# Kernel tuning notes

Hardware: AMD Instinct MI355X
Metric: run time of the kernel (lower is better)

The kernel has to match this reference:

```python
import jax, jax.numpy as jnp
import numpy as np

B, N, H, O = 262144, 64, 256, 64
MAX_ITER = 30
TOL = 1e-7
NU = 1.0


def setup_inputs() -> dict:
    key = jax.random.key(0)
    kx, kr, k1, k2, k3, k4 = jax.random.split(key, 6)
    x = jax.random.normal(kx, (B, N), dtype=jnp.float32) * 3.0
    r = jax.random.uniform(kr, (N,), dtype=jnp.float32) + 0.5  # positive rates in [0.5, 1.5)
    # MLP params (torch Linear: y = x @ W.T + b), Kaiming-ish scaling
    W1 = jax.random.normal(k1, (H, N), dtype=jnp.float32) * (1.0 / np.sqrt(N))
    b1 = jax.random.normal(k2, (H,), dtype=jnp.float32) * 0.01
    W2 = jax.random.normal(k3, (O, H), dtype=jnp.float32) * (1.0 / np.sqrt(H))
    b2 = jax.random.normal(k4, (O,), dtype=jnp.float32) * 0.01
    return {"x": x, "r": r, "W1": W1, "b1": b1, "W2": W2, "b2": b2}


def _solve_s(x, r):
    """Vectorized Newton solve of sum_i e^{-2 r_i s} x_i^2 = 1 per sample.

    Replicates solve_s_single: s starts at 0, up to MAX_ITER Newton steps,
    frozen once |F(s)| < TOL; all-zero samples return s = 0.
    """
    x2 = x * x  # [B, N]
    zero_mask = jnp.all(jnp.abs(x) <= 1e-12, axis=1)  # torch.allclose(x, 0, atol=1e-12)

    def body(_, s):
        e = jnp.exp(-2.0 * r[None, :] * s[:, None])        # [B, N]
        val = jnp.sum(e * x2, axis=1) - 1.0                # F(s)     [B]
        dval = jnp.sum(-2.0 * r[None, :] * e * x2, axis=1) # F'(s)    [B]
        safe_d = jnp.where(dval == 0.0, 1.0, dval)
        step = val / safe_d
        step = jnp.where((jnp.abs(val) < TOL) | zero_mask, 0.0, step)
        return s - step

    s0 = jnp.zeros(x.shape[0], dtype=x.dtype)
    return jax.lax.fori_loop(0, MAX_ITER, body, s0)


def reference(x, r, W1, b1, W2, b2):
    S = _solve_s(x, r)[:, None]                 # [B, 1], detached in torch (built via .item())
    S = jax.lax.stop_gradient(S)
    x_sphere = x * jnp.exp(-r[None, :] * S)     # d(-s) x
    h = jnp.maximum(x_sphere @ W1.T + b1, 0.0)  # [B, H]
    mlp_out = h @ W2.T + b2                     # [B, O]
    return mlp_out * jnp.exp(NU * S)
```

## Files before the change

kernel.cpp:

```cpp
#include <hip/hip_runtime.h>

typedef __attribute__((ext_vector_type(8))) short short8;
typedef __attribute__((ext_vector_type(4))) float floatx4;

static __device__ __forceinline__ unsigned short f2bf(float f) {
    unsigned u = __float_as_uint(f);
    u += 0x7FFFu + ((u >> 16) & 1u);
    return (unsigned short)(u >> 16);
}

__global__ __launch_bounds__(256) void convert_w_k(const float* __restrict__ W1,
                                                   const float* __restrict__ W2,
                                                   unsigned short* __restrict__ w1b,
                                                   unsigned short* __restrict__ w2b) {
    int i = blockIdx.x * 256 + threadIdx.x;
    w1b[i] = f2bf(W1[i]);
    w2b[i] = f2bf(W2[i]);
}

__global__ __launch_bounds__(256) void newton_k(const float* __restrict__ x,
                                                const float* __restrict__ r,
                                                unsigned short* __restrict__ xs,
                                                float* __restrict__ scl) {
    int tid = blockIdx.x * 256 + threadIdx.x;
    int sample = tid >> 2;
    int part = tid & 3;

    const float4* x4 = (const float4*)(x + (size_t)sample * 64 + part * 16);
    const float4* r4 = (const float4*)(r + part * 16);
    float xv[16], rr[16], x2[16], rx2[16];
#pragma unroll
    for (int j = 0; j < 4; ++j) {
        float4 a = x4[j];
        float4 b = r4[j];
        xv[4 * j + 0] = a.x; xv[4 * j + 1] = a.y; xv[4 * j + 2] = a.z; xv[4 * j + 3] = a.w;
        rr[4 * j + 0] = b.x; rr[4 * j + 1] = b.y; rr[4 * j + 2] = b.z; rr[4 * j + 3] = b.w;
    }

    float sum0 = 0.f, sumr = 0.f;
    int nz = 0;
#pragma unroll
    for (int j = 0; j < 16; ++j) {
        x2[j] = xv[j] * xv[j];
        rx2[j] = rr[j] * x2[j];
        sum0 += x2[j];
        sumr += rx2[j];
        nz |= (fabsf(xv[j]) > 1e-12f) ? 1 : 0;
    }
    sum0 += __shfl_xor(sum0, 1); sum0 += __shfl_xor(sum0, 2);
    sumr += __shfl_xor(sumr, 1); sumr += __shfl_xor(sumr, 2);
    nz   |= __shfl_xor(nz, 1);   nz   |= __shfl_xor(nz, 2);

    float s = 0.f;
    if (nz) {
        s = __logf(sum0) * sum0 / (2.f * sumr);
#pragma unroll 1
        for (int it = 0; it < 11; ++it) {
            float m2s = -2.f * s;
            float v = 0.f, dv = 0.f;
#pragma unroll
            for (int j = 0; j < 16; ++j) {
                float e = __expf(m2s * rr[j]);
                v = fmaf(e, x2[j], v);
                dv = fmaf(e, rx2[j], dv);
            }
            v += __shfl_xor(v, 1);   v += __shfl_xor(v, 2);
            dv += __shfl_xor(dv, 1); dv += __shfl_xor(dv, 2);
            float val = v - 1.f;
            s += val / (2.f * dv);
        }
    }

    unsigned up[8];
#pragma unroll
    for (int j = 0; j < 8; ++j) {
        float a = xv[2 * j] * __expf(-s * rr[2 * j]);
        float b = xv[2 * j + 1] * __expf(-s * rr[2 * j + 1]);
        up[j] = (unsigned)f2bf(a) | ((unsigned)f2bf(b) << 16);
    }
    uint4* dst = (uint4*)(xs + (size_t)sample * 64 + part * 16);
    dst[0] = make_uint4(up[0], up[1], up[2], up[3]);
    dst[1] = make_uint4(up[4], up[5], up[6], up[7]);
    if (part == 0) scl[sample] = __expf(s);
}

__global__ __launch_bounds__(256, 2) void mlp_k(const unsigned short* __restrict__ xs,
                                                const float* __restrict__ scl,
                                                const unsigned short* __restrict__ w1b,
                                                const unsigned short* __restrict__ w2b,
                                                const float* __restrict__ b1,
                                                const float* __restrict__ b2,
                                                float* __restrict__ out,
                                                int tiles_per_block) {
    __shared__ unsigned short sW1[256 * 64];
    __shared__ unsigned short sW2[64 * 256];
    __shared__ unsigned short sH[64 * 64];

    int tid = threadIdx.x;

    const uint4* w1u = (const uint4*)w1b;
#pragma unroll
    for (int c = 0; c < 8; ++c) {
        int g = tid + c * 256;
        int row = g >> 3, ch = g & 7;
        *(uint4*)&sW1[row * 64 + (ch ^ (row & 7)) * 8] = w1u[g];
    }
    const uint4* w2u = (const uint4*)w2b;
#pragma unroll
    for (int c = 0; c < 8; ++c) {
        int g = tid + c * 256;
        int row = g >> 5, ch = g & 31;
        *(uint4*)&sW2[row * 256 + (ch ^ (row & 7)) * 8] = w2u[g];
    }
    __syncthreads();

    int wave = tid >> 6, lane = tid & 63;
    int q = lane >> 4, l16 = lane & 15;
    int sx = l16 & 7;

    float bias1[16];
#pragma unroll
    for (int n = 0; n < 16; ++n) bias1[n] = b1[n * 16 + l16];
    float bias2[4];
#pragma unroll
    for (int n = 0; n < 4; ++n) bias2[n] = b2[n * 16 + l16];

    for (int tt = 0; tt < tiles_per_block; ++tt) {
        size_t m0 = ((size_t)blockIdx.x * tiles_per_block + tt) * 64;
        int myrow = wave * 16 + l16;

        const short8* xrow = (const short8*)(xs + (m0 + myrow) * 64);
        short8 a0 = xrow[q];
        short8 a1 = xrow[q + 4];
        float sc[4];
#pragma unroll
        for (int reg = 0; reg < 4; ++reg) sc[reg] = scl[m0 + wave * 16 + q * 4 + reg];

        floatx4 oacc[4];
#pragma unroll
        for (int n = 0; n < 4; ++n) oacc[n] = (floatx4){0.f, 0.f, 0.f, 0.f};

#pragma unroll
        for (int hc = 0; hc < 4; ++hc) {
#pragma unroll
            for (int n = 0; n < 4; ++n) {
                int hcol = hc * 4 + n;
                int row = hcol * 16 + l16;
                short8 wb0 = *(const short8*)&sW1[row * 64 + (q ^ sx) * 8];
                short8 wb1 = *(const short8*)&sW1[row * 64 + ((q + 4) ^ sx) * 8];
                floatx4 acc = {0.f, 0.f, 0.f, 0.f};
                acc = __builtin_amdgcn_mfma_f32_16x16x32_bf16(a0, wb0, acc, 0, 0, 0);
                acc = __builtin_amdgcn_mfma_f32_16x16x32_bf16(a1, wb1, acc, 0, 0, 0);
                float bias = bias1[hcol];
#pragma unroll
                for (int reg = 0; reg < 4; ++reg) {
                    float h = acc[reg] + bias;
                    h = h > 0.f ? h : 0.f;
                    int rr = wave * 16 + q * 4 + reg;
                    int E = n * 16 + l16;
                    sH[rr * 64 + (((E >> 3) ^ (rr & 7)) * 8) + (E & 7)] = f2bf(h);
                }
            }
            short8 ha0 = *(const short8*)&sH[myrow * 64 + (q ^ sx) * 8];
            short8 ha1 = *(const short8*)&sH[myrow * 64 + ((q + 4) ^ sx) * 8];
#pragma unroll
            for (int n = 0; n < 4; ++n) {
                int row = n * 16 + l16;
                short8 wb0 = *(const short8*)&sW2[row * 256 + (hc * 8 + (q ^ sx)) * 8];
                short8 wb1 = *(const short8*)&sW2[row * 256 + (hc * 8 + ((q + 4) ^ sx)) * 8];
                oacc[n] = __builtin_amdgcn_mfma_f32_16x16x32_bf16(ha0, wb0, oacc[n], 0, 0, 0);
                oacc[n] = __builtin_amdgcn_mfma_f32_16x16x32_bf16(ha1, wb1, oacc[n], 0, 0, 0);
            }
        }
#pragma unroll
        for (int n = 0; n < 4; ++n) {
#pragma unroll
            for (int reg = 0; reg < 4; ++reg) {
                float o = (oacc[n][reg] + bias2[n]) * sc[reg];
                out[(m0 + wave * 16 + q * 4 + reg) * 64 + n * 16 + l16] = o;
            }
        }
    }
}

extern "C" void kernel_launch(void* const* d_in, const int* in_sizes, int n_in,
                              void* d_out, int out_size, void* d_ws, size_t ws_size,
                              hipStream_t stream) {
    const float* x  = (const float*)d_in[0];
    const float* r  = (const float*)d_in[1];
    const float* W1 = (const float*)d_in[2];
    const float* b1 = (const float*)d_in[3];
    const float* W2 = (const float*)d_in[4];
    const float* b2 = (const float*)d_in[5];
    float* out = (float*)d_out;
    int B = in_sizes[0] / 64;

    char* ws = (char*)d_ws;
    unsigned short* w1b = (unsigned short*)ws;
    unsigned short* w2b = (unsigned short*)(ws + 32768);
    float* scl = (float*)(ws + 65536);
    unsigned short* xs = (unsigned short*)(ws + 65536 + (size_t)B * 4);

    convert_w_k<<<64, 256, 0, stream>>>(W1, W2, w1b, w2b);
    newton_k<<<B / 64, 256, 0, stream>>>(x, r, xs, scl);

    int tiles = B / 64;
    int blocks = 512;
    int tpb = tiles / blocks;
    mlp_k<<<blocks, 256, 0, stream>>>(xs, scl, w1b, w2b, b1, b2, out, tpb);
}
```

Baseline: 168.5 us.

## Fuse Newton solve into MLP kernel and drop bf16 intermediate buffer

Merges the per-sample Newton solve into the MLP kernel. Each wave now computes the scaled input rows for its own 16 samples, writes them to a shared-memory tile that is reused for the hidden activations, and passes the exp(s) scale through lane shuffles. This removes the global write and re-read of the bf16 intermediate and the scale array, plus one kernel launch. To cut shared-memory use and allow 4 blocks per CU (grid doubled to 1024), W2 is no longer staged in LDS and is read from global memory through the cache instead. The risk is extra cache traffic and latency on every W2 fragment load inside the inner loop.

```diff
diff --git a/kernel.cpp b/kernel.cpp
--- a/kernel.cpp
+++ b/kernel.cpp
@@ -18,83 +18,16 @@
     w2b[i] = f2bf(W2[i]);
 }
 
-__global__ __launch_bounds__(256) void newton_k(const float* __restrict__ x,
-                                                const float* __restrict__ r,
-                                                unsigned short* __restrict__ xs,
-                                                float* __restrict__ scl) {
-    int tid = blockIdx.x * 256 + threadIdx.x;
-    int sample = tid >> 2;
-    int part = tid & 3;
-
-    const float4* x4 = (const float4*)(x + (size_t)sample * 64 + part * 16);
-    const float4* r4 = (const float4*)(r + part * 16);
-    float xv[16], rr[16], x2[16], rx2[16];
-#pragma unroll
-    for (int j = 0; j < 4; ++j) {
-        float4 a = x4[j];
-        float4 b = r4[j];
-        xv[4 * j + 0] = a.x; xv[4 * j + 1] = a.y; xv[4 * j + 2] = a.z; xv[4 * j + 3] = a.w;
-        rr[4 * j + 0] = b.x; rr[4 * j + 1] = b.y; rr[4 * j + 2] = b.z; rr[4 * j + 3] = b.w;
-    }
-
-    float sum0 = 0.f, sumr = 0.f;
-    int nz = 0;
-#pragma unroll
-    for (int j = 0; j < 16; ++j) {
-        x2[j] = xv[j] * xv[j];
-        rx2[j] = rr[j] * x2[j];
-        sum0 += x2[j];
-        sumr += rx2[j];
-        nz |= (fabsf(xv[j]) > 1e-12f) ? 1 : 0;
-    }
-    sum0 += __shfl_xor(sum0, 1); sum0 += __shfl_xor(sum0, 2);
-    sumr += __shfl_xor(sumr, 1); sumr += __shfl_xor(sumr, 2);
-    nz   |= __shfl_xor(nz, 1);   nz   |= __shfl_xor(nz, 2);
-
-    float s = 0.f;
-    if (nz) {
-        s = __logf(sum0) * sum0 / (2.f * sumr);
-#pragma unroll 1
-        for (int it = 0; it < 11; ++it) {
-            float m2s = -2.f * s;
-            float v = 0.f, dv = 0.f;
-#pragma unroll
-            for (int j = 0; j < 16; ++j) {
-                float e = __expf(m2s * rr[j]);
-                v = fmaf(e, x2[j], v);
-                dv = fmaf(e, rx2[j], dv);
-            }
-            v += __shfl_xor(v, 1);   v += __shfl_xor(v, 2);
-            dv += __shfl_xor(dv, 1); dv += __shfl_xor(dv, 2);
-            float val = v - 1.f;
-            s += val / (2.f * dv);
-        }
-    }
-
-    unsigned up[8];
-#pragma unroll
-    for (int j = 0; j < 8; ++j) {
-        float a = xv[2 * j] * __expf(-s * rr[2 * j]);
-        float b = xv[2 * j + 1] * __expf(-s * rr[2 * j + 1]);
-        up[j] = (unsigned)f2bf(a) | ((unsigned)f2bf(b) << 16);
-    }
-    uint4* dst = (uint4*)(xs + (size_t)sample * 64 + part * 16);
-    dst[0] = make_uint4(up[0], up[1], up[2], up[3]);
-    dst[1] = make_uint4(up[4], up[5], up[6], up[7]);
-    if (part == 0) scl[sample] = __expf(s);
-}
-
-__global__ __launch_bounds__(256, 2) void mlp_k(const unsigned short* __restrict__ xs,
-                                                const float* __restrict__ scl,
-                                                const unsigned short* __restrict__ w1b,
-                                                const unsigned short* __restrict__ w2b,
-                                                const float* __restrict__ b1,
-                                                const float* __restrict__ b2,
-                                                float* __restrict__ out,
-                                                int tiles_per_block) {
+__global__ __launch_bounds__(256, 4) void fused_k(const float* __restrict__ x,
+                                                  const float* __restrict__ r,
+                                                  const unsigned short* __restrict__ w1b,
+                                                  const unsigned short* __restrict__ w2b,
+                                                  const float* __restrict__ b1,
+                                                  const float* __restrict__ b2,
+                                                  float* __restrict__ out,
+                                                  int tiles_per_block) {
     __shared__ unsigned short sW1[256 * 64];
-    __shared__ unsigned short sW2[64 * 256];
-    __shared__ unsigned short sH[64 * 64];
+    __shared__ unsigned short sXH[64 * 64];
 
     int tid = threadIdx.x;
 
@@ -105,18 +38,21 @@
         int row = g >> 3, ch = g & 7;
         *(uint4*)&sW1[row * 64 + (ch ^ (row & 7)) * 8] = w1u[g];
     }
-    const uint4* w2u = (const uint4*)w2b;
-#pragma unroll
-    for (int c = 0; c < 8; ++c) {
-        int g = tid + c * 256;
-        int row = g >> 5, ch = g & 31;
-        *(uint4*)&sW2[row * 256 + (ch ^ (row & 7)) * 8] = w2u[g];
-    }
     __syncthreads();
 
     int wave = tid >> 6, lane = tid & 63;
     int q = lane >> 4, l16 = lane & 15;
     int sx = l16 & 7;
+    int part = tid & 3;
+    int rloc = tid >> 2;
+
+    const float4* r4 = (const float4*)(r + part * 16);
+    float rr[16];
+#pragma unroll
+    for (int j = 0; j < 4; ++j) {
+        float4 b = r4[j];
+        rr[4 * j + 0] = b.x; rr[4 * j + 1] = b.y; rr[4 * j + 2] = b.z; rr[4 * j + 3] = b.w;
+    }
 
     float bias1[16];
 #pragma unroll
@@ -125,16 +61,69 @@
 #pragma unroll
     for (int n = 0; n < 4; ++n) bias2[n] = b2[n * 16 + l16];
 
+    int myrow = wave * 16 + l16;
+    int kx = rloc & 7;
+
     for (int tt = 0; tt < tiles_per_block; ++tt) {
         size_t m0 = ((size_t)blockIdx.x * tiles_per_block + tt) * 64;
-        int myrow = wave * 16 + l16;
 
-        const short8* xrow = (const short8*)(xs + (m0 + myrow) * 64);
-        short8 a0 = xrow[q];
-        short8 a1 = xrow[q + 4];
+        const float4* x4 = (const float4*)(x + (m0 + rloc) * 64 + part * 16);
+        float xv[16], x2[16], rx2[16];
+        float sum0 = 0.f, sumr = 0.f;
+        int nz = 0;
+#pragma unroll
+        for (int j = 0; j < 4; ++j) {
+            float4 a = x4[j];
+            xv[4 * j + 0] = a.x; xv[4 * j + 1] = a.y; xv[4 * j + 2] = a.z; xv[4 * j + 3] = a.w;
+        }
+#pragma unroll
+        for (int j = 0; j < 16; ++j) {
+            x2[j] = xv[j] * xv[j];
+            rx2[j] = rr[j] * x2[j];
+            sum0 += x2[j];
+            sumr += rx2[j];
+            nz |= (fabsf(xv[j]) > 1e-12f) ? 1 : 0;
+        }
+        sum0 += __shfl_xor(sum0, 1); sum0 += __shfl_xor(sum0, 2);
+        sumr += __shfl_xor(sumr, 1); sumr += __shfl_xor(sumr, 2);
+        nz   |= __shfl_xor(nz, 1);   nz   |= __shfl_xor(nz, 2);
+
+        float s = 0.f;
+        if (nz) {
+            s = __logf(sum0) * sum0 / (2.f * sumr);
+#pragma unroll 1
+            for (int it = 0; it < 11; ++it) {
+                float m2s = -2.f * s;
+                float v = 0.f, dv = 0.f;
+#pragma unroll
+                for (int j = 0; j < 16; ++j) {
+                    float e = __expf(m2s * rr[j]);
+                    v = fmaf(e, x2[j], v);
+                    dv = fmaf(e, rx2[j], dv);
+                }
+                v += __shfl_xor(v, 1);   v += __shfl_xor(v, 2);
+                dv += __shfl_xor(dv, 1); dv += __shfl_xor(dv, 2);
+                float val = v - 1.f;
+                s += val / (2.f * dv);
+            }
+        }
+        float es = __expf(s);
+
+        unsigned up[8];
+#pragma unroll
+        for (int j = 0; j < 8; ++j) {
+            float a = xv[2 * j] * __expf(-s * rr[2 * j]);
+            float b = xv[2 * j + 1] * __expf(-s * rr[2 * j + 1]);
+            up[j] = (unsigned)f2bf(a) | ((unsigned)f2bf(b) << 16);
+        }
+        *(uint4*)&sXH[rloc * 64 + ((2 * part) ^ kx) * 8] = make_uint4(up[0], up[1], up[2], up[3]);
+        *(uint4*)&sXH[rloc * 64 + ((2 * part + 1) ^ kx) * 8] = make_uint4(up[4], up[5], up[6], up[7]);
+
+        short8 a0 = *(const short8*)&sXH[myrow * 64 + (q ^ sx) * 8];
+        short8 a1 = *(const short8*)&sXH[myrow * 64 + ((q + 4) ^ sx) * 8];
         float sc[4];
 #pragma unroll
-        for (int reg = 0; reg < 4; ++reg) sc[reg] = scl[m0 + wave * 16 + q * 4 + reg];
+        for (int reg = 0; reg < 4; ++reg) sc[reg] = __shfl(es, (q * 4 + reg) * 4);
 
         floatx4 oacc[4];
 #pragma unroll
@@ -156,18 +145,18 @@
                 for (int reg = 0; reg < 4; ++reg) {
                     float h = acc[reg] + bias;
                     h = h > 0.f ? h : 0.f;
-                    int rr = wave * 16 + q * 4 + reg;
+                    int rw = wave * 16 + q * 4 + reg;
                     int E = n * 16 + l16;
-                    sH[rr * 64 + (((E >> 3) ^ (rr & 7)) * 8) + (E & 7)] = f2bf(h);
+                    sXH[rw * 64 + (((E >> 3) ^ (rw & 7)) * 8) + (E & 7)] = f2bf(h);
                 }
             }
-            short8 ha0 = *(const short8*)&sH[myrow * 64 + (q ^ sx) * 8];
-            short8 ha1 = *(const short8*)&sH[myrow * 64 + ((q + 4) ^ sx) * 8];
+            short8 ha0 = *(const short8*)&sXH[myrow * 64 + (q ^ sx) * 8];
+            short8 ha1 = *(const short8*)&sXH[myrow * 64 + ((q + 4) ^ sx) * 8];
 #pragma unroll
             for (int n = 0; n < 4; ++n) {
                 int row = n * 16 + l16;
-                short8 wb0 = *(const short8*)&sW2[row * 256 + (hc * 8 + (q ^ sx)) * 8];
-                short8 wb1 = *(const short8*)&sW2[row * 256 + (hc * 8 + ((q + 4) ^ sx)) * 8];
+                short8 wb0 = *(const short8*)(w2b + row * 256 + hc * 64 + q * 8);
+                short8 wb1 = *(const short8*)(w2b + row * 256 + hc * 64 + 32 + q * 8);
                 oacc[n] = __builtin_amdgcn_mfma_f32_16x16x32_bf16(ha0, wb0, oacc[n], 0, 0, 0);
                 oacc[n] = __builtin_amdgcn_mfma_f32_16x16x32_bf16(ha1, wb1, oacc[n], 0, 0, 0);
             }
@@ -198,14 +187,11 @@
     char* ws = (char*)d_ws;
     unsigned short* w1b = (unsigned short*)ws;
     unsigned short* w2b = (unsigned short*)(ws + 32768);
-    float* scl = (float*)(ws + 65536);
-    unsigned short* xs = (unsigned short*)(ws + 65536 + (size_t)B * 4);
 
     convert_w_k<<<64, 256, 0, stream>>>(W1, W2, w1b, w2b);
-    newton_k<<<B / 64, 256, 0, stream>>>(x, r, xs, scl);
 
     int tiles = B / 64;
-    int blocks = 512;
+    int blocks = 1024;
     int tpb = tiles / blocks;
-    mlp_k<<<blocks, 256, 0, stream>>>(xs, scl, w1b, w2b, b1, b2, out, tpb);
+    fused_k<<<blocks, 256, 0, stream>>>(x, r, w1b, w2b, b1, b2, out, tpb);
 }
```

Result: slower. 277.7 us (+64.8%).
